# Performance work log

Hardware: AMD Instinct MI355X
Metric: run time of the kernel (lower is better)

Reference implementation:

```python
import jax, jax.numpy as jnp
import numpy as np

B, S, D = 1, 2048, 2048
H, HD = 16, 128  # n_heads, head_dim
ROPE_BASE = 100000.0


def setup_inputs() -> dict:
    key = jax.random.key(0)
    k0, k1, k2 = jax.random.split(key, 3)
    x = jax.random.normal(k0, (B, S, D), jnp.float32)
    # real RoPE table: (seq_len, head_dim//2, 2) holding (cos, sin)
    inv_freq = 1.0 / (ROPE_BASE ** (np.arange(0, HD, 2, dtype=np.float64) / HD))
    t = np.arange(S, dtype=np.float64)[:, None] * inv_freq[None, :]
    freqs_cis = jnp.asarray(np.stack([np.cos(t), np.sin(t)], axis=-1), jnp.float32)
    input_pos = jnp.arange(S, dtype=jnp.int32)
    Wqkv = jax.random.normal(k1, (D, 3 * D), jnp.float32) * (D ** -0.5)
    bqkv = jnp.zeros((3 * D,), jnp.float32)
    Wdense = jax.random.normal(k2, (D, D), jnp.float32) * (D ** -0.5)
    bdense = jnp.zeros((D,), jnp.float32)
    return {"x": x, "freqs_cis": freqs_cis, "input_pos": input_pos,
            "Wqkv": Wqkv, "bqkv": bqkv, "Wdense": Wdense, "bdense": bdense}


def apply_rotary_emb(x, freqs_cis):
    # x: [B, S, H, HD]; freqs_cis: [S, HD//2, 2]
    xs = x.reshape(*x.shape[:-1], -1, 2)  # [B,S,H,HD/2,2]
    fc = freqs_cis.reshape(1, xs.shape[1], 1, xs.shape[3], 2)
    out = jnp.stack([
        xs[..., 0] * fc[..., 0] - xs[..., 1] * fc[..., 1],
        xs[..., 1] * fc[..., 0] + xs[..., 0] * fc[..., 1],
    ], axis=-1)
    return out.reshape(x.shape).astype(x.dtype)


def reference(x, freqs_cis, input_pos, Wqkv, bqkv, Wdense, bdense):
    b, s, d = x.shape
    qkv = x @ Wqkv + bqkv                      # fused QKV projection
    q, k, v = jnp.split(qkv, 3, axis=-1)
    q = q.reshape(b, s, H, HD)
    k = k.reshape(b, s, H, HD)
    v = v.reshape(b, s, H, HD)
    q = apply_rotary_emb(q, freqs_cis)
    k = apply_rotary_emb(k, freqs_cis)
    # KV-cache update (cache batch = 1, max_seq = context_length)
    k_cache = jnp.zeros((1, S, H, HD), jnp.float32)
    v_cache = jnp.zeros((1, S, H, HD), jnp.float32)
    k_full = k_cache.at[:, input_pos].set(k)
    v_full = v_cache.at[:, input_pos].set(v)
    # causal SDPA in [B, H, S, HD] layout
    qh = q.transpose(0, 2, 1, 3)
    kh = k_full.transpose(0, 2, 1, 3)
    vh = v_full.transpose(0, 2, 1, 3)
    scale = HD ** -0.5
    scores = jnp.einsum('bhqd,bhkd->bhqk', qh, kh) * scale  # [B,H,S,S]
    causal = jnp.tril(jnp.ones((s, S), dtype=bool))
    scores = jnp.where(causal, scores, jnp.finfo(scores.dtype).min)
    attn = jax.nn.softmax(scores, axis=-1)
    ctx = jnp.einsum('bhqk,bhkd->bhqd', attn, vh)
    ctx = ctx.transpose(0, 2, 1, 3).reshape(b, s, d)
    return ctx @ Wdense + bdense
```

## Files before the change

kernel.cpp:

```cpp
#include <hip/hip_runtime.h>

#define S 2048
#define D 2048
#define H 16
#define HD 128
#define N3 6144

typedef __attribute__((ext_vector_type(8))) _Float16 f16x8;
typedef __attribute__((ext_vector_type(4))) float f32x4;
typedef unsigned short ushort_t;
typedef unsigned int uint_t;

__device__ __forceinline__ ushort_t f16_rne(float f) {
    _Float16 h = (_Float16)f;
    return __builtin_bit_cast(ushort_t, h);
}
__device__ __forceinline__ float f16_f32(ushort_t u) {
    return (float)__builtin_bit_cast(_Float16, u);
}

__global__ __launch_bounds__(256) void convert_f16_kernel(
    const float* __restrict__ in, ushort_t* __restrict__ hi)
{
    const int i = blockIdx.x * 256 + threadIdx.x;
    float4 v = ((const float4*)in)[i];
    ((ushort4*)hi)[i] = make_ushort4(f16_rne(v.x), f16_rne(v.y),
                                     f16_rne(v.z), f16_rne(v.w));
}

__global__ __launch_bounds__(256) void convert_t_kernel(
    const float* __restrict__ in, ushort_t* __restrict__ hi,
    int Kdim, int Ndim)
{
    __shared__ float tile[32][33];
    const int k0 = blockIdx.x * 32, n0 = blockIdx.y * 32;
    const int tx = threadIdx.x & 31, ty = threadIdx.x >> 5;
    #pragma unroll
    for (int r = 0; r < 4; r++)
        tile[ty + r * 8][tx] = in[(size_t)(k0 + ty + r * 8) * Ndim + n0 + tx];
    __syncthreads();
    const int n  = threadIdx.x >> 3;
    const int kc = (threadIdx.x & 7) * 4;
    const float v0 = tile[kc + 0][n], v1 = tile[kc + 1][n];
    const float v2 = tile[kc + 2][n], v3 = tile[kc + 3][n];
    const size_t off = (size_t)(n0 + n) * Kdim + k0 + kc;
    *(ushort4*)&hi[off] = make_ushort4(f16_rne(v0), f16_rne(v1),
                                       f16_rne(v2), f16_rne(v3));
}

__device__ __forceinline__ void gload16(const ushort_t* g, ushort_t* l) {
    __builtin_amdgcn_global_load_lds(
        (const __attribute__((address_space(1))) unsigned int*)g,
        (__attribute__((address_space(3))) unsigned int*)l, 16, 0, 0);
}

#define BK 32
#define TILE_ELEMS (128 * BK)

__device__ __forceinline__ void mm_core_1t(
    const ushort_t* __restrict__ Agh,
    const ushort_t* __restrict__ Bgh,
    const int K, ushort_t* lds, const int t, f32x4 (&acc)[4][4])
{
    const int lane = t & 63;
    const int wv   = t >> 6;
    const int lrow = lane >> 2;
    const int lk   = (lane & 3) * 8;
    const int quad = lane >> 4;
    const int lr   = lane & 15;
    const int wm   = (wv & 1) * 64;
    const int wn   = (wv >> 1) * 64;

    const int r0  = wv * 16;
    const int lo0 = r0 * BK;
    const int lo1 = (r0 + 64) * BK;

    auto stage = [&](int k0, int buf) {
        ushort_t* base = lds + buf * 2 * TILE_ELEMS;
        ushort_t* As_h = base;
        ushort_t* Bs_h = base + TILE_ELEMS;
        const size_t go0 = (size_t)(r0 + lrow) * K + k0 + lk;
        const size_t go1 = (size_t)(r0 + 64 + lrow) * K + k0 + lk;
        gload16(Agh + go0, As_h + lo0);
        gload16(Agh + go1, As_h + lo1);
        gload16(Bgh + go0, Bs_h + lo0);
        gload16(Bgh + go1, Bs_h + lo1);
    };

    stage(0, 0);

    const int niter = K / BK;
    for (int it = 0; it < niter; it++) {
        const int cur = it & 1;
        __syncthreads();

        if (it + 1 < niter) stage((it + 1) * BK, cur ^ 1);

        ushort_t* base = lds + cur * 2 * TILE_ELEMS;
        ushort_t* As_h = base;
        ushort_t* Bs_h = base + TILE_ELEMS;

        f16x8 af[4], bf[4];
        #pragma unroll
        for (int i = 0; i < 4; i++) {
            af[i] = *(const f16x8*)&As_h[(wm + i * 16 + lr) * BK + quad * 8];
            bf[i] = *(const f16x8*)&Bs_h[(wn + i * 16 + lr) * BK + quad * 8];
        }
        #pragma unroll
        for (int mt = 0; mt < 4; mt++)
            #pragma unroll
            for (int nt = 0; nt < 4; nt++)
                acc[mt][nt] = __builtin_amdgcn_mfma_f32_16x16x32_f16(
                    af[mt], bf[nt], acc[mt][nt], 0, 0, 0);
    }
}

__global__ __launch_bounds__(256) void gemm_qkv_mfma(
    const ushort_t* __restrict__ xh,
    const ushort_t* __restrict__ Wth,
    const float* __restrict__ bias, const float* __restrict__ freqs,
    const int* __restrict__ input_pos,
    ushort_t* __restrict__ qhg, ushort_t* __restrict__ khg,
    ushort_t* __restrict__ vhg)
{
    __shared__ ushort_t lds[2 * 2 * TILE_ELEMS];
    const int t = threadIdx.x;
    const int col0 = blockIdx.x * 128;
    const int row0 = blockIdx.y * 128;

    f32x4 acc[4][4] = {};
    mm_core_1t(xh + (size_t)row0 * D,
               Wth + (size_t)col0 * D,
               D, lds, t, acc);

    const int lane = t & 63;
    const int quad = lane >> 4;
    const int lr   = lane & 15;
    const int wm = ((t >> 6) & 1) * 64;
    const int wn = ((t >> 6) >> 1) * 64;

    const int which = col0 >> 11;
    const int hh = (col0 & 2047) >> 7;

    if (which == 2) {
        ushort_t* vh_b = vhg + (size_t)hh * HD * S;
        #pragma unroll
        for (int nt = 0; nt < 4; nt++) {
            const int d = wn + nt * 16 + lr;
            const float bsc = bias[col0 + d];
            #pragma unroll
            for (int mt = 0; mt < 4; mt++) {
                #pragma unroll
                for (int reg = 0; reg < 4; reg++) {
                    const int m = row0 + wm + mt * 16 + quad * 4 + reg;
                    const float v = acc[mt][nt][reg] + bsc;
                    const int pos = input_pos[m];
                    vh_b[(size_t)d * S + pos] = f16_rne(v);
                }
            }
        }
    } else {
        ushort_t* oh_b = ((which == 0) ? qhg : khg) + (size_t)hh * S * HD;
        #pragma unroll
        for (int nt = 0; nt < 4; nt++) {
            const int d = wn + nt * 16 + lr;
            const float bsc = bias[col0 + d];
            #pragma unroll
            for (int mt = 0; mt < 4; mt++) {
                #pragma unroll
                for (int reg = 0; reg < 4; reg++) {
                    const int m = row0 + wm + mt * 16 + quad * 4 + reg;
                    const float v = acc[mt][nt][reg] + bsc;
                    const float* fc = &freqs[((size_t)m * 64 + (d >> 1)) * 2];
                    const float c = fc[0], s = fc[1];
                    const float p = __shfl_xor(v, 1);
                    const float o = (d & 1) ? (v * c + p * s) : (v * c - p * s);
                    const ushort_t hv = f16_rne(o);
                    const int hp = __shfl_xor((int)hv, 1);
                    if (!(d & 1)) {
                        const int srow = (which == 0) ? m : input_pos[m];
                        *(uint_t*)&oh_b[(size_t)srow * HD + d] =
                            (uint_t)hv | ((uint_t)hp << 16);
                    }
                }
            }
        }
    }
}

__global__ __launch_bounds__(256, 2) void attn_mfma_kernel(
    const ushort_t* __restrict__ qhg, const ushort_t* __restrict__ khg,
    const ushort_t* __restrict__ vhg,
    float* __restrict__ Opart, float* __restrict__ MLpart)
{
    __shared__ ushort_t Khs[2][4096];
    __shared__ ushort_t Vhs[2][4096];
    __shared__ ushort_t Ps[64 * 32];

    const int bi   = blockIdx.x;
    const int h    = (bi & 7) + 8 * ((bi >> 3) & 1);
    const int half = (bi >> 4) & 1;
    const int qi   = bi >> 5;
    const int r = (h & 8) ? qi : (31 - qi);
    const int q0 = r * 64;
    const int nhalf = r + 1;
    const int kt0 = half * nhalf;
    const int kt1 = kt0 + nhalf;
    const int t = threadIdx.x;
    const int w = t >> 6, lane = t & 63;
    const int lr = lane & 15, quad = lane >> 4;

    const size_t qrow = (size_t)h * S + q0 + w * 16 + lr;
    f16x8 qf[4];
    #pragma unroll
    for (int ks = 0; ks < 4; ks++)
        qf[ks] = *(const f16x8*)&qhg[qrow * HD + ks * 32 + quad * 8];

    const ushort_t* kh_b = khg + (size_t)h * S * HD;
    const ushort_t* vh_b = vhg + (size_t)h * HD * S;

    const int keyq = lane >> 2;
    const int sub  = lane & 3;

    auto stage = [&](int kt, int buf) {
        const int k0 = kt * 32;
        #pragma unroll
        for (int hf = 0; hf < 2; hf++) {
            const size_t ksrc = (size_t)(k0 + hf * 16 + keyq) * HD + w * 32 + sub * 8;
            gload16(kh_b + ksrc, &Khs[buf][w * 1024 + hf * 512]);
            const int dim = w * 32 + hf * 16 + keyq;
            const size_t vsrc = (size_t)dim * S + k0 + sub * 8;
            gload16(vh_b + vsrc, &Vhs[buf][(w * 32 + hf * 16) * 32]);
        }
    };

    f32x4 O[8] = {};
    f32x4 Ol = {0.f, 0.f, 0.f, 0.f};
    float mrow[4];
    #pragma unroll
    for (int rr = 0; rr < 4; rr++) mrow[rr] = -1e30f;

    f16x8 onesv;
    #pragma unroll
    for (int i = 0; i < 8; i++) onesv[i] = (_Float16)1.0f;

    const float kSc = 0.08838834764831845f * 1.4426950408889634f;

    stage(kt0, 0);

    for (int kt = kt0; kt < kt1; kt++) {
        const int k0 = kt * 32;
        const int cur = (kt - kt0) & 1;
        __syncthreads();

        if (kt + 1 < kt1) stage(kt + 1, cur ^ 1);

        f32x4 sa[2];
        #pragma unroll
        for (int nt = 0; nt < 2; nt++) {
            f32x4 s = {0.f, 0.f, 0.f, 0.f};
            #pragma unroll
            for (int ks = 0; ks < 4; ks++) {
                f16x8 kf = *(const f16x8*)&Khs[cur][ks * 1024 + (nt * 16 + lr) * 32 + quad * 8];
                s = __builtin_amdgcn_mfma_f32_16x16x32_f16(qf[ks], kf, s, 0, 0, 0);
            }
            sa[nt] = s;
        }

        const int rowbase = q0 + w * 16 + quad * 4;
        const bool need_mask = (k0 + 31) > (q0 + w * 16);
        float alpha[4], pv0[4], pv1[4];
        #pragma unroll
        for (int rr = 0; rr < 4; rr++) {
            float z0 = sa[0][rr] * kSc;
            float z1 = sa[1][rr] * kSc;
            if (need_mask) {
                const int rowg = rowbase + rr;
                if (k0 + lr > rowg)      z0 = -1e30f;
                if (k0 + 16 + lr > rowg) z1 = -1e30f;
            }
            float rm = fmaxf(z0, z1);
            #pragma unroll
            for (int off = 1; off < 16; off <<= 1)
                rm = fmaxf(rm, __shfl_xor(rm, off));
            const float nm = fmaxf(mrow[rr], rm);
            alpha[rr] = exp2f(mrow[rr] - nm);
            pv0[rr] = exp2f(z0 - nm);
            pv1[rr] = exp2f(z1 - nm);
            mrow[rr] = nm;
        }

        #pragma unroll
        for (int rr = 0; rr < 4; rr++) {
            const int prow = (w * 16 + quad * 4 + rr) * 32;
            Ps[prow + lr]      = f16_rne(pv0[rr]);
            Ps[prow + 16 + lr] = f16_rne(pv1[rr]);
        }

        #pragma unroll
        for (int nt = 0; nt < 8; nt++)
            #pragma unroll
            for (int rr = 0; rr < 4; rr++)
                O[nt][rr] *= alpha[rr];
        #pragma unroll
        for (int rr = 0; rr < 4; rr++)
            Ol[rr] *= alpha[rr];
        const f16x8 pf = *(const f16x8*)&Ps[(w * 16 + lr) * 32 + quad * 8];
        #pragma unroll
        for (int nt = 0; nt < 8; nt++) {
            f16x8 vf = *(const f16x8*)&Vhs[cur][(nt * 16 + lr) * 32 + quad * 8];
            O[nt] = __builtin_amdgcn_mfma_f32_16x16x32_f16(pf, vf, O[nt], 0, 0, 0);
        }
        Ol = __builtin_amdgcn_mfma_f32_16x16x32_f16(pf, onesv, Ol, 0, 0, 0);
    }

    float* Ob = Opart + (size_t)bi * 64 * 128;
    #pragma unroll
    for (int rr = 0; rr < 4; rr++) {
        const int row = w * 16 + quad * 4 + rr;
        #pragma unroll
        for (int nt = 0; nt < 8; nt++)
            Ob[(size_t)row * 128 + nt * 16 + lr] = O[nt][rr];
        if (lr == 0) {
            MLpart[(size_t)bi * 128 + row * 2 + 0] = mrow[rr];
            MLpart[(size_t)bi * 128 + row * 2 + 1] = Ol[rr];
        }
    }
}

__global__ __launch_bounds__(128) void attn_combine_kernel(
    const float* __restrict__ Opart, const float* __restrict__ MLpart,
    ushort_t* __restrict__ ctxh)
{
    const int qt = blockIdx.x;
    const int h  = blockIdx.y;
    const int t  = threadIdx.x;
    const int b0 = h | (qt << 5);
    const int b1 = b0 | (1 << 4);
    const int r = (h & 8) ? qt : (31 - qt);
    const int q0 = r * 64;

    __shared__ float sc[64][2];
    if (t < 64) {
        const float m0 = MLpart[(size_t)b0 * 128 + t * 2 + 0];
        const float l0 = MLpart[(size_t)b0 * 128 + t * 2 + 1];
        const float m1 = MLpart[(size_t)b1 * 128 + t * 2 + 0];
        const float l1 = MLpart[(size_t)b1 * 128 + t * 2 + 1];
        const float m = fmaxf(m0, m1);
        const float a0 = exp2f(m0 - m), a1 = exp2f(m1 - m);
        const float inv = 1.0f / (l0 * a0 + l1 * a1);
        sc[t][0] = a0 * inv;
        sc[t][1] = a1 * inv;
    }
    __syncthreads();

    const float* O0 = Opart + (size_t)b0 * 64 * 128;
    const float* O1 = Opart + (size_t)b1 * 64 * 128;
    for (int row = 0; row < 64; row++) {
        const float o = O0[(size_t)row * 128 + t] * sc[row][0] +
                        O1[(size_t)row * 128 + t] * sc[row][1];
        ctxh[(size_t)(q0 + row) * D + h * HD + t] = f16_rne(o);
    }
}

__global__ __launch_bounds__(256) void gemm_dense_mfma(
    const ushort_t* __restrict__ Ah,
    const ushort_t* __restrict__ Wth,
    const float* __restrict__ bias, float* __restrict__ out)
{
    __shared__ ushort_t lds[2 * 2 * TILE_ELEMS];
    const int t = threadIdx.x;
    const int col0 = blockIdx.x * 128;
    const int row0 = blockIdx.y * 128;

    f32x4 acc[4][4] = {};
    mm_core_1t(Ah + (size_t)row0 * D,
               Wth + (size_t)col0 * D,
               D, lds, t, acc);

    const int lane = t & 63;
    const int quad = lane >> 4;
    const int lr   = lane & 15;
    const int wm = ((t >> 6) & 1) * 64;
    const int wn = ((t >> 6) >> 1) * 64;

    #pragma unroll
    for (int nt = 0; nt < 4; nt++) {
        const int n = col0 + wn + nt * 16 + lr;
        const float bsc = bias[n];
        #pragma unroll
        for (int mt = 0; mt < 4; mt++) {
            #pragma unroll
            for (int reg = 0; reg < 4; reg++) {
                const int m = row0 + wm + mt * 16 + quad * 4 + reg;
                const float o = acc[mt][nt][reg] + bsc;
                const float po = __shfl_xor(o, 1);
                if (!(n & 1))
                    *(float2*)&out[(size_t)m * D + n] = make_float2(o, po);
            }
        }
    }
}

__global__ __launch_bounds__(256) void gemm_qkv_kernel(
    const float* __restrict__ x, const float* __restrict__ W,
    const float* __restrict__ bias, const float* __restrict__ freqs,
    const int* __restrict__ input_pos,
    float* __restrict__ qb, float* __restrict__ kb, float* __restrict__ vb)
{
    __shared__ float As[16][68];
    __shared__ float Bs[16][64];
    const int bx = blockIdx.x;
    const int by = blockIdx.y;
    const int tid = threadIdx.x;
    const int tx = tid & 15, ty = tid >> 4;
    const int row0 = by * 64, col0 = bx * 64;
    const int am = tid >> 2;
    const int ak = (tid & 3) * 4;
    const int bk = tid >> 4;
    const int bn = (tid & 15) * 4;
    float acc[4][4] = {};
    for (int k0 = 0; k0 < D; k0 += 16) {
        float4 av = *(const float4*)&x[(size_t)(row0 + am) * D + k0 + ak];
        float4 bv = *(const float4*)&W[(size_t)(k0 + bk) * N3 + col0 + bn];
        __syncthreads();
        As[ak + 0][am] = av.x; As[ak + 1][am] = av.y;
        As[ak + 2][am] = av.z; As[ak + 3][am] = av.w;
        *(float4*)&Bs[bk][bn] = bv;
        __syncthreads();
        #pragma unroll
        for (int k = 0; k < 16; k++) {
            float4 a4 = *(const float4*)&As[k][ty * 4];
            float4 b4 = *(const float4*)&Bs[k][tx * 4];
            float a[4] = {a4.x, a4.y, a4.z, a4.w};
            float b[4] = {b4.x, b4.y, b4.z, b4.w};
            #pragma unroll
            for (int r = 0; r < 4; r++)
                #pragma unroll
                for (int c = 0; c < 4; c++)
                    acc[r][c] += a[r] * b[c];
        }
    }
    const int j0 = col0 + tx * 4;
    const int which = j0 >> 11;
    const int hh = (j0 & 2047) >> 7;
    const int d0 = j0 & 127;
    const float bv0 = bias[j0 + 0], bv1 = bias[j0 + 1];
    const float bv2 = bias[j0 + 2], bv3 = bias[j0 + 3];
    #pragma unroll
    for (int r = 0; r < 4; r++) {
        const int grow = row0 + ty * 4 + r;
        float v0 = acc[r][0] + bv0, v1 = acc[r][1] + bv1;
        float v2 = acc[r][2] + bv2, v3 = acc[r][3] + bv3;
        if (which == 2) {
            const int pos = input_pos[grow];
            float4 o4 = make_float4(v0, v1, v2, v3);
            *(float4*)&vb[((size_t)hh * S + pos) * HD + d0] = o4;
        } else {
            const float* fc = &freqs[((size_t)grow * 64 + (d0 >> 1)) * 2];
            float c0 = fc[0], s0 = fc[1], c1 = fc[2], s1 = fc[3];
            float o0 = v0 * c0 - v1 * s0, o1 = v1 * c0 + v0 * s0;
            float o2 = v2 * c1 - v3 * s1, o3 = v3 * c1 + v2 * s1;
            float4 o4 = make_float4(o0, o1, o2, o3);
            if (which == 0) {
                *(float4*)&qb[((size_t)hh * S + grow) * HD + d0] = o4;
            } else {
                const int pos = input_pos[grow];
                *(float4*)&kb[((size_t)hh * S + pos) * HD + d0] = o4;
            }
        }
    }
}

#define BQ 64
#define ABK 32
#define QSTR 132
#define KVSTR 132
#define PSTR 68

__global__ __launch_bounds__(256) void attn_kernel(
    const float* __restrict__ qb, const float* __restrict__ kb,
    const float* __restrict__ vb, float* __restrict__ ctx)
{
    __shared__ float Qs[BQ * QSTR];
    __shared__ float KV[ABK * KVSTR];
    __shared__ float Psf[ABK * PSTR];

    const int pa = blockIdx.x;
    const int h  = blockIdx.y;
    const int t  = threadIdx.x;
    const int ty = t >> 4, tx = t & 15;
    const int i0  = ty * 4;
    const int j0  = tx * 2;
    const int dd0 = tx * 8;
    const int lr = t >> 3;
    const int lc = (t & 7) * 4;

    const float* kbase = kb + (size_t)h * S * HD;
    const float* vbase = vb + (size_t)h * S * HD;
    const float kSc = 0.08838834764831845f * 1.4426950408889634f;

    for (int ph = 0; ph < 2; ph++) {
        const int r = (ph == 0) ? pa : 31 - pa;
        const int q0 = r * BQ;
        const int ntiles = 2 * r + 2;

        #pragma unroll
        for (int pp = 0; pp < 2; pp++) {
            const int iq = lr + pp * 32;
            const float* src = qb + ((size_t)h * S + q0 + iq) * HD;
            #pragma unroll
            for (int ch = 0; ch < 4; ch++)
                *(float4*)&Qs[iq * QSTR + lc + ch * 32] =
                    *(const float4*)&src[lc + ch * 32];
        }

        float O[4][8] = {};
        float m[4], l[4];
        #pragma unroll
        for (int rr = 0; rr < 4; rr++) { m[rr] = -1e30f; l[rr] = 0.f; }

        float4 kpref[4];
        #pragma unroll
        for (int ch = 0; ch < 4; ch++)
            kpref[ch] = *(const float4*)&kbase[(size_t)lr * HD + lc + ch * 32];

        __syncthreads();

        for (int kt = 0; kt < ntiles; kt++) {
            const int k0 = kt * ABK;

            #pragma unroll
            for (int ch = 0; ch < 4; ch++)
                *(float4*)&KV[lr * KVSTR + lc + ch * 32] = kpref[ch];
            __syncthreads();

            float4 vpref[4];
            #pragma unroll
            for (int ch = 0; ch < 4; ch++)
                vpref[ch] = *(const float4*)&vbase[(size_t)(k0 + lr) * HD + lc + ch * 32];

            float acc[4][2] = {};
            #pragma unroll 4
            for (int d0 = 0; d0 < HD; d0 += 4) {
                float4 ka = *(const float4*)&KV[(j0 + 0) * KVSTR + d0];
                float4 kb4 = *(const float4*)&KV[(j0 + 1) * KVSTR + d0];
                #pragma unroll
                for (int rr = 0; rr < 4; rr++) {
                    float4 q4 = *(const float4*)&Qs[(i0 + rr) * QSTR + d0];
                    acc[rr][0] += q4.x * ka.x + q4.y * ka.y + q4.z * ka.z + q4.w * ka.w;
                    acc[rr][1] += q4.x * kb4.x + q4.y * kb4.y + q4.z * kb4.z + q4.w * kb4.w;
                }
            }

            const bool need_mask = (k0 + ABK - 1) > q0;
            float p[4][2], alpha[4];
            #pragma unroll
            for (int rr = 0; rr < 4; rr++) {
                float z0 = acc[rr][0] * kSc;
                float z1 = acc[rr][1] * kSc;
                if (need_mask) {
                    if (k0 + j0 + 0 > q0 + i0 + rr) z0 = -1e30f;
                    if (k0 + j0 + 1 > q0 + i0 + rr) z1 = -1e30f;
                }
                float rmax = fmaxf(z0, z1);
                #pragma unroll
                for (int off = 1; off < 16; off <<= 1)
                    rmax = fmaxf(rmax, __shfl_xor(rmax, off, 16));
                const float nm = fmaxf(m[rr], rmax);
                alpha[rr] = exp2f(m[rr] - nm);
                p[rr][0] = exp2f(z0 - nm);
                p[rr][1] = exp2f(z1 - nm);
                float ts = p[rr][0] + p[rr][1];
                #pragma unroll
                for (int off = 1; off < 16; off <<= 1)
                    ts += __shfl_xor(ts, off, 16);
                l[rr] = l[rr] * alpha[rr] + ts;
                m[rr] = nm;
            }
            __syncthreads();

            #pragma unroll
            for (int ch = 0; ch < 4; ch++)
                *(float4*)&KV[lr * KVSTR + lc + ch * 32] = vpref[ch];
            *(float4*)&Psf[(j0 + 0) * PSTR + i0] =
                make_float4(p[0][0], p[1][0], p[2][0], p[3][0]);
            *(float4*)&Psf[(j0 + 1) * PSTR + i0] =
                make_float4(p[0][1], p[1][1], p[2][1], p[3][1]);
            if (kt + 1 < ntiles) {
                #pragma unroll
                for (int ch = 0; ch < 4; ch++)
                    kpref[ch] = *(const float4*)&kbase[(size_t)(k0 + ABK + lr) * HD + lc + ch * 32];
            }
            __syncthreads();

            #pragma unroll
            for (int rr = 0; rr < 4; rr++)
                #pragma unroll
                for (int c = 0; c < 8; c++)
                    O[rr][c] *= alpha[rr];
            #pragma unroll 4
            for (int j = 0; j < ABK; j++) {
                float4 pj = *(const float4*)&Psf[j * PSTR + i0];
                float4 v0 = *(const float4*)&KV[j * KVSTR + dd0];
                float4 v1 = *(const float4*)&KV[j * KVSTR + dd0 + 4];
                const float pr[4] = {pj.x, pj.y, pj.z, pj.w};
                const float vv[8] = {v0.x, v0.y, v0.z, v0.w, v1.x, v1.y, v1.z, v1.w};
                #pragma unroll
                for (int rr = 0; rr < 4; rr++)
                    #pragma unroll
                    for (int c = 0; c < 8; c++)
                        O[rr][c] += pr[rr] * vv[c];
            }
            __syncthreads();
        }

        #pragma unroll
        for (int rr = 0; rr < 4; rr++) {
            const float inv = 1.0f / l[rr];
            const int qg = q0 + i0 + rr;
            float4 o0 = make_float4(O[rr][0] * inv, O[rr][1] * inv,
                                    O[rr][2] * inv, O[rr][3] * inv);
            float4 o1 = make_float4(O[rr][4] * inv, O[rr][5] * inv,
                                    O[rr][6] * inv, O[rr][7] * inv);
            float* dst = &ctx[((size_t)qg * H + h) * HD + dd0];
            *(float4*)&dst[0] = o0;
            *(float4*)&dst[4] = o1;
        }
        __syncthreads();
    }
}

__global__ __launch_bounds__(256) void gemm_dense_kernel(
    const float* __restrict__ A, const float* __restrict__ W,
    const float* __restrict__ bias, float* __restrict__ out)
{
    __shared__ float As[16][68];
    __shared__ float Bs[16][64];
    const int bx = blockIdx.x;
    const int by = blockIdx.y;
    const int tid = threadIdx.x;
    const int tx = tid & 15, ty = tid >> 4;
    const int row0 = by * 64, col0 = bx * 64;
    const int am = tid >> 2;
    const int ak = (tid & 3) * 4;
    const int bk = tid >> 4;
    const int bn = (tid & 15) * 4;
    float acc[4][4] = {};
    for (int k0 = 0; k0 < D; k0 += 16) {
        float4 av = *(const float4*)&A[(size_t)(row0 + am) * D + k0 + ak];
        float4 bv = *(const float4*)&W[(size_t)(k0 + bk) * D + col0 + bn];
        __syncthreads();
        As[ak + 0][am] = av.x; As[ak + 1][am] = av.y;
        As[ak + 2][am] = av.z; As[ak + 3][am] = av.w;
        *(float4*)&Bs[bk][bn] = bv;
        __syncthreads();
        #pragma unroll
        for (int k = 0; k < 16; k++) {
            float4 a4 = *(const float4*)&As[k][ty * 4];
            float4 b4 = *(const float4*)&Bs[k][tx * 4];
            float a[4] = {a4.x, a4.y, a4.z, a4.w};
            float b[4] = {b4.x, b4.y, b4.z, b4.w};
            #pragma unroll
            for (int r = 0; r < 4; r++)
                #pragma unroll
                for (int c = 0; c < 4; c++)
                    acc[r][c] += a[r] * b[c];
        }
    }
    const int j0 = col0 + tx * 4;
    const float bv0 = bias[j0 + 0], bv1 = bias[j0 + 1];
    const float bv2 = bias[j0 + 2], bv3 = bias[j0 + 3];
    #pragma unroll
    for (int r = 0; r < 4; r++) {
        const int grow = row0 + ty * 4 + r;
        float4 o4 = make_float4(acc[r][0] + bv0, acc[r][1] + bv1,
                                acc[r][2] + bv2, acc[r][3] + bv3);
        *(float4*)&out[(size_t)grow * D + j0] = o4;
    }
}

extern "C" void kernel_launch(void* const* d_in, const int* in_sizes, int n_in,
                              void* d_out, int out_size, void* d_ws, size_t ws_size,
                              hipStream_t stream) {
    const float* x      = (const float*)d_in[0];
    const float* freqs  = (const float*)d_in[1];
    const int*   pos    = (const int*)d_in[2];
    const float* Wqkv   = (const float*)d_in[3];
    const float* bqkv   = (const float*)d_in[4];
    const float* Wdense = (const float*)d_in[5];
    const float* bdense = (const float*)d_in[6];
    float* out = (float*)d_out;

    const size_t nSD = (size_t)S * D;
    const size_t nW1 = (size_t)D * N3;
    const size_t nOP = (size_t)1024 * 64 * 128;
    const size_t nML = (size_t)1024 * 128;

    const size_t needed =
        (6 * nSD + nW1) * sizeof(ushort_t) + (nOP + nML) * sizeof(float);

    if (ws_size >= needed) {
        ushort_t* qh   = (ushort_t*)d_ws;
        ushort_t* kh   = qh + nSD;
        ushort_t* vh   = kh + nSD;
        ushort_t* ctxh = vh + nSD;
        ushort_t* xh   = ctxh + nSD;
        ushort_t* Wth  = xh + nSD;
        ushort_t* Wdth = Wth + nW1;
        float* Opart = (float*)(Wdth + nSD);
        float* MLpart = Opart + nOP;

        convert_f16_kernel<<<nSD / 4 / 256, 256, 0, stream>>>(x, xh);
        dim3 gt1(D / 32, N3 / 32);
        convert_t_kernel<<<gt1, 256, 0, stream>>>(Wqkv, Wth, D, N3);
        dim3 gt2(D / 32, D / 32);
        convert_t_kernel<<<gt2, 256, 0, stream>>>(Wdense, Wdth, D, D);

        dim3 g1(N3 / 128, S / 128);
        gemm_qkv_mfma<<<g1, 256, 0, stream>>>(xh, Wth, bqkv, freqs,
                                              pos, qh, kh, vh);
        attn_mfma_kernel<<<1024, 256, 0, stream>>>(qh, kh, vh,
                                                   Opart, MLpart);
        dim3 gc(32, H);
        attn_combine_kernel<<<gc, 128, 0, stream>>>(Opart, MLpart, ctxh);
        dim3 g3(D / 128, S / 128);
        gemm_dense_mfma<<<g3, 256, 0, stream>>>(ctxh, Wdth, bdense, out);
    } else {
        float* qb  = (float*)d_ws;
        float* kb  = qb + (size_t)H * S * HD;
        float* vb  = kb + (size_t)H * S * HD;
        float* ctx = vb + (size_t)H * S * HD;
        dim3 g1(N3 / 64, S / 64);
        gemm_qkv_kernel<<<g1, 256, 0, stream>>>(x, Wqkv, bqkv, freqs, pos, qb, kb, vb);
        dim3 g2(16, H);
        attn_kernel<<<g2, 256, 0, stream>>>(qb, kb, vb, ctx);
        dim3 g3(D / 64, S / 64);
        gemm_dense_kernel<<<g3, 256, 0, stream>>>(ctx, Wdense, bdense, out);
    }
}
```

Measured before the change: 362.4 us.

## Rewrite QKV GEMM with 256x256 tiles and explicit software-pipelined staging

Replaces the 128x128, 256-thread QKV projection GEMM with a 256x256-tile, 512-thread kernel. It uses a BK=64 K-step split into two halves, a double-buffered 128KB LDS, async global-to-LDS loads issued several phases ahead, and hand-placed vmcnt/lgkmcnt waits, barriers and s_setprio around the MFMA bursts. The goal is to raise arithmetic intensity per block and overlap global loads with MFMA work. The trade-off is that the grid shrinks to 192 blocks, fewer than the CU count, and the large LDS footprint limits each CU to one resident block. The bias and RoPE epilogue and the scatter to Q/K/V are kept as before, adapted to the larger tile.

```diff
diff --git a/kernel.cpp b/kernel.cpp
--- a/kernel.cpp
+++ b/kernel.cpp
@@ -54,6 +54,161 @@
         (__attribute__((address_space(3))) unsigned int*)l, 16, 0, 0);
 }
 
+__device__ __forceinline__ void vwait8() { asm volatile("s_waitcnt vmcnt(8)" ::: "memory"); }
+__device__ __forceinline__ void vwait4() { asm volatile("s_waitcnt vmcnt(4)" ::: "memory"); }
+__device__ __forceinline__ void vwait0() { asm volatile("s_waitcnt vmcnt(0)" ::: "memory"); }
+__device__ __forceinline__ void lwait0() { asm volatile("s_waitcnt lgkmcnt(0)" ::: "memory"); }
+
+#define QNT 32
+
+__global__ __launch_bounds__(512, 2) void gemm_qkv_mfma(
+    const ushort_t* __restrict__ xh,
+    const ushort_t* __restrict__ Wth,
+    const float* __restrict__ bias, const float* __restrict__ freqs,
+    const int* __restrict__ input_pos,
+    ushort_t* __restrict__ qhg, ushort_t* __restrict__ khg,
+    ushort_t* __restrict__ vhg)
+{
+    __shared__ ushort_t lds[65536];
+    const int t = threadIdx.x;
+    const int w = t >> 6, lane = t & 63;
+    const int lr = lane & 15, quad = lane >> 4;
+    const int wm = (w >> 2) * 128;
+    const int wn = (w & 3) * 64;
+
+    const int col0 = blockIdx.x * 256;
+    const int row0 = blockIdx.y * 256;
+    const ushort_t* At = xh + (size_t)row0 * D;
+    const ushort_t* Bt = Wth + (size_t)col0 * D;
+
+    const int srow = lane >> 2;
+    const int scol = (lane & 3) * 8;
+    const size_t goff0 = (size_t)((0 * 8 + w) * 16 + srow) * D + scol;
+    const size_t goff1 = (size_t)((1 * 8 + w) * 16 + srow) * D + scol;
+    const int ldst0 = (0 * 8 + w) * 512;
+    const int ldst1 = (1 * 8 + w) * 512;
+
+    auto stage = [&](int j, int Tt) {
+        const ushort_t* gb = (j & 1) ? Bt : At;
+        const int off = Tt * 64 + (j >> 1) * 32;
+        ushort_t* dst = lds + (Tt & 1) * 32768 + j * 8192;
+        gload16(gb + goff0 + off, dst + ldst0);
+        gload16(gb + goff1 + off, dst + ldst1);
+    };
+
+    f32x4 acc[8][4] = {};
+    const int aro = (wm + lr) * 32 + quad * 8;
+    const int bro = 8192 + (wn + lr) * 32 + quad * 8;
+
+    stage(0, 0); stage(1, 0); stage(2, 0); stage(3, 0);
+    stage(0, 1); stage(1, 1);
+    vwait4();
+    __builtin_amdgcn_sched_barrier(0);
+    __builtin_amdgcn_s_barrier();
+
+    f16x8 af[4], bf[4];
+
+#define QPH(kk, mtg, RDB, DOSTAGE, SJ, ST, WAITN)                          \
+    {                                                                      \
+        const ushort_t* base = lds + (T & 1) * 32768 + (kk) * 16384;       \
+        _Pragma("unroll")                                                  \
+        for (int i = 0; i < 4; i++)                                        \
+            af[i] = *(const f16x8*)&base[aro + ((mtg) * 4 + i) * 512];     \
+        if (RDB) {                                                         \
+            _Pragma("unroll")                                              \
+            for (int n = 0; n < 4; n++)                                    \
+                bf[n] = *(const f16x8*)&base[bro + n * 512];               \
+        }                                                                  \
+        if (DOSTAGE) stage(SJ, ST);                                        \
+        __builtin_amdgcn_s_barrier();                                      \
+        lwait0();                                                          \
+        __builtin_amdgcn_sched_barrier(0);                                 \
+        __builtin_amdgcn_s_setprio(1);                                     \
+        _Pragma("unroll")                                                  \
+        for (int i = 0; i < 4; i++)                                        \
+            _Pragma("unroll")                                              \
+            for (int n = 0; n < 4; n++)                                    \
+                acc[(mtg) * 4 + i][n] =                                    \
+                    __builtin_amdgcn_mfma_f32_16x16x32_f16(                \
+                        af[i], bf[n], acc[(mtg) * 4 + i][n], 0, 0, 0);     \
+        __builtin_amdgcn_s_setprio(0);                                     \
+        WAITN;                                                             \
+        __builtin_amdgcn_s_barrier();                                      \
+    }
+
+    for (int T = 0; T < QNT - 2; T++) {
+        QPH(0, 0, true,  true, 2, T + 1, );
+        QPH(0, 1, false, true, 3, T + 1, vwait8());
+        QPH(1, 0, true,  true, 0, T + 2, );
+        QPH(1, 1, false, true, 1, T + 2, vwait8());
+    }
+    {
+        const int T = QNT - 2;
+        QPH(0, 0, true,  true,  2, T + 1, );
+        QPH(0, 1, false, true,  3, T + 1, vwait8());
+        QPH(1, 0, true,  false, 0, 0, );
+        QPH(1, 1, false, false, 0, 0, vwait4());
+    }
+    {
+        const int T = QNT - 1;
+        QPH(0, 0, true,  false, 0, 0, );
+        QPH(0, 1, false, false, 0, 0, vwait0());
+        QPH(1, 0, true,  false, 0, 0, );
+        QPH(1, 1, false, false, 0, 0, );
+    }
+#undef QPH
+
+    const int which = col0 >> 11;
+    if (which == 2) {
+        #pragma unroll
+        for (int nt = 0; nt < 4; nt++) {
+            const int c = col0 + wn + nt * 16 + lr;
+            const int hh = (c & 2047) >> 7;
+            const int d = c & 127;
+            ushort_t* vh_b = vhg + (size_t)hh * HD * S;
+            const float bsc = bias[c];
+            #pragma unroll
+            for (int mt = 0; mt < 8; mt++) {
+                #pragma unroll
+                for (int reg = 0; reg < 4; reg++) {
+                    const int m = row0 + wm + mt * 16 + quad * 4 + reg;
+                    const float v = acc[mt][nt][reg] + bsc;
+                    vh_b[(size_t)d * S + input_pos[m]] = f16_rne(v);
+                }
+            }
+        }
+    } else {
+        ushort_t* ohg = (which == 0) ? qhg : khg;
+        #pragma unroll
+        for (int nt = 0; nt < 4; nt++) {
+            const int c = col0 + wn + nt * 16 + lr;
+            const int hh = (c & 2047) >> 7;
+            const int d = c & 127;
+            ushort_t* oh_b = ohg + (size_t)hh * S * HD;
+            const float bsc = bias[c];
+            #pragma unroll
+            for (int mt = 0; mt < 8; mt++) {
+                #pragma unroll
+                for (int reg = 0; reg < 4; reg++) {
+                    const int m = row0 + wm + mt * 16 + quad * 4 + reg;
+                    const float v = acc[mt][nt][reg] + bsc;
+                    const float* fc = &freqs[((size_t)m * 64 + (d >> 1)) * 2];
+                    const float cc = fc[0], ss = fc[1];
+                    const float p = __shfl_xor(v, 1);
+                    const float o = (d & 1) ? (v * cc + p * ss) : (v * cc - p * ss);
+                    const ushort_t hv = f16_rne(o);
+                    const int hp = __shfl_xor((int)hv, 1);
+                    if (!(d & 1)) {
+                        const int srowg = (which == 0) ? m : input_pos[m];
+                        *(uint_t*)&oh_b[(size_t)srowg * HD + d] =
+                            (uint_t)hv | ((uint_t)hp << 16);
+                    }
+                }
+            }
+        }
+    }
+}
+
 #define BK 32
 #define TILE_ELEMS (128 * BK)
 
@@ -112,79 +267,6 @@
             for (int nt = 0; nt < 4; nt++)
                 acc[mt][nt] = __builtin_amdgcn_mfma_f32_16x16x32_f16(
                     af[mt], bf[nt], acc[mt][nt], 0, 0, 0);
-    }
-}
-
-__global__ __launch_bounds__(256) void gemm_qkv_mfma(
-    const ushort_t* __restrict__ xh,
-    const ushort_t* __restrict__ Wth,
-    const float* __restrict__ bias, const float* __restrict__ freqs,
-    const int* __restrict__ input_pos,
-    ushort_t* __restrict__ qhg, ushort_t* __restrict__ khg,
-    ushort_t* __restrict__ vhg)
-{
-    __shared__ ushort_t lds[2 * 2 * TILE_ELEMS];
-    const int t = threadIdx.x;
-    const int col0 = blockIdx.x * 128;
-    const int row0 = blockIdx.y * 128;
-
-    f32x4 acc[4][4] = {};
-    mm_core_1t(xh + (size_t)row0 * D,
-               Wth + (size_t)col0 * D,
-               D, lds, t, acc);
-
-    const int lane = t & 63;
-    const int quad = lane >> 4;
-    const int lr   = lane & 15;
-    const int wm = ((t >> 6) & 1) * 64;
-    const int wn = ((t >> 6) >> 1) * 64;
-
-    const int which = col0 >> 11;
-    const int hh = (col0 & 2047) >> 7;
-
-    if (which == 2) {
-        ushort_t* vh_b = vhg + (size_t)hh * HD * S;
-        #pragma unroll
-        for (int nt = 0; nt < 4; nt++) {
-            const int d = wn + nt * 16 + lr;
-            const float bsc = bias[col0 + d];
-            #pragma unroll
-            for (int mt = 0; mt < 4; mt++) {
-                #pragma unroll
-                for (int reg = 0; reg < 4; reg++) {
-                    const int m = row0 + wm + mt * 16 + quad * 4 + reg;
-                    const float v = acc[mt][nt][reg] + bsc;
-                    const int pos = input_pos[m];
-                    vh_b[(size_t)d * S + pos] = f16_rne(v);
-                }
-            }
-        }
-    } else {
-        ushort_t* oh_b = ((which == 0) ? qhg : khg) + (size_t)hh * S * HD;
-        #pragma unroll
-        for (int nt = 0; nt < 4; nt++) {
-            const int d = wn + nt * 16 + lr;
-            const float bsc = bias[col0 + d];
-            #pragma unroll
-            for (int mt = 0; mt < 4; mt++) {
-                #pragma unroll
-                for (int reg = 0; reg < 4; reg++) {
-                    const int m = row0 + wm + mt * 16 + quad * 4 + reg;
-                    const float v = acc[mt][nt][reg] + bsc;
-                    const float* fc = &freqs[((size_t)m * 64 + (d >> 1)) * 2];
-                    const float c = fc[0], s = fc[1];
-                    const float p = __shfl_xor(v, 1);
-                    const float o = (d & 1) ? (v * c + p * s) : (v * c - p * s);
-                    const ushort_t hv = f16_rne(o);
-                    const int hp = __shfl_xor((int)hv, 1);
-                    if (!(d & 1)) {
-                        const int srow = (which == 0) ? m : input_pos[m];
-                        *(uint_t*)&oh_b[(size_t)srow * HD + d] =
-                            (uint_t)hv | ((uint_t)hp << 16);
-                    }
-                }
-            }
-        }
     }
 }
 
@@ -717,8 +799,8 @@
         dim3 gt2(D / 32, D / 32);
         convert_t_kernel<<<gt2, 256, 0, stream>>>(Wdense, Wdth, D, D);
 
-        dim3 g1(N3 / 128, S / 128);
-        gemm_qkv_mfma<<<g1, 256, 0, stream>>>(xh, Wth, bqkv, freqs,
+        dim3 g1(N3 / 256, S / 256);
+        gemm_qkv_mfma<<<g1, 512, 0, stream>>>(xh, Wth, bqkv, freqs,
                                               pos, qh, kh, vh);
         attn_mfma_kernel<<<1024, 256, 0, stream>>>(qh, kh, vh,
                                                    Opart, MLpart);
```

Measured after the change: 354.8 us. 1.02x faster.

## Replace GEMM core with deeper multi-stage pipelined LDS prefetch and explicit waitcnts

Applied to the files above, without the earlier changes.

The GEMM inner loop used by the QKV and dense projections is rewritten. It now uses a 64-wide K tile split into two 32-wide phases, with prefetch running two tiles ahead across a 64KB LDS double buffer. Explicit vmcnt/lgkmcnt waits, raw s_barrier calls, sched_barrier and setprio around the MFMA block aim to overlap global-to-LDS loads with compute and to cut the full __syncthreads cost. Launch bounds now request 2 blocks per CU. The risk is that 64KB of LDS per block limits occupancy, and the hand-placed waits must be exactly right to avoid races.

```diff
diff --git a/kernel.cpp b/kernel.cpp
--- a/kernel.cpp
+++ b/kernel.cpp
@@ -54,68 +54,94 @@
         (__attribute__((address_space(3))) unsigned int*)l, 16, 0, 0);
 }
 
-#define BK 32
-#define TILE_ELEMS (128 * BK)
-
-__device__ __forceinline__ void mm_core_1t(
-    const ushort_t* __restrict__ Agh,
-    const ushort_t* __restrict__ Bgh,
-    const int K, ushort_t* lds, const int t, f32x4 (&acc)[4][4])
-{
-    const int lane = t & 63;
-    const int wv   = t >> 6;
-    const int lrow = lane >> 2;
-    const int lk   = (lane & 3) * 8;
-    const int quad = lane >> 4;
-    const int lr   = lane & 15;
-    const int wm   = (wv & 1) * 64;
-    const int wn   = (wv >> 1) * 64;
-
-    const int r0  = wv * 16;
-    const int lo0 = r0 * BK;
-    const int lo1 = (r0 + 64) * BK;
-
-    auto stage = [&](int k0, int buf) {
-        ushort_t* base = lds + buf * 2 * TILE_ELEMS;
-        ushort_t* As_h = base;
-        ushort_t* Bs_h = base + TILE_ELEMS;
-        const size_t go0 = (size_t)(r0 + lrow) * K + k0 + lk;
-        const size_t go1 = (size_t)(r0 + 64 + lrow) * K + k0 + lk;
-        gload16(Agh + go0, As_h + lo0);
-        gload16(Agh + go1, As_h + lo1);
-        gload16(Bgh + go0, Bs_h + lo0);
-        gload16(Bgh + go1, Bs_h + lo1);
+__device__ __forceinline__ void vwait8() { asm volatile("s_waitcnt vmcnt(8)" ::: "memory"); }
+__device__ __forceinline__ void vwait4() { asm volatile("s_waitcnt vmcnt(4)" ::: "memory"); }
+__device__ __forceinline__ void vwait0() { asm volatile("s_waitcnt vmcnt(0)" ::: "memory"); }
+__device__ __forceinline__ void lwait0() { asm volatile("s_waitcnt lgkmcnt(0)" ::: "memory"); }
+
+#define QNT 32
+
+__device__ __forceinline__ void mm_core_8ph(
+    const ushort_t* __restrict__ At, const ushort_t* __restrict__ Bt,
+    ushort_t* lds, const int t, f32x4 (&acc)[4][4])
+{
+    const int w = t >> 6, lane = t & 63;
+    const int lr = lane & 15, quad = lane >> 4;
+    const int wm = (w & 1) * 64;
+    const int wn = (w >> 1) * 64;
+
+    const int srow = lane >> 2;
+    const int scol = (lane & 3) * 8;
+    const size_t goff0 = (size_t)(w * 16 + srow) * D + scol;
+    const size_t goff1 = goff0 + (size_t)64 * D;
+    const int ldst0 = w * 512;
+    const int ldst1 = 2048 + w * 512;
+
+    auto stage = [&](int j, int Tt) {
+        const ushort_t* gb = (j & 1) ? Bt : At;
+        const size_t off = (size_t)Tt * 64 + (j >> 1) * 32;
+        ushort_t* dst = lds + (Tt & 1) * 16384 + j * 4096;
+        gload16(gb + goff0 + off, dst + ldst0);
+        gload16(gb + goff1 + off, dst + ldst1);
     };
 
-    stage(0, 0);
-
-    const int niter = K / BK;
-    for (int it = 0; it < niter; it++) {
-        const int cur = it & 1;
-        __syncthreads();
-
-        if (it + 1 < niter) stage((it + 1) * BK, cur ^ 1);
-
-        ushort_t* base = lds + cur * 2 * TILE_ELEMS;
-        ushort_t* As_h = base;
-        ushort_t* Bs_h = base + TILE_ELEMS;
-
-        f16x8 af[4], bf[4];
-        #pragma unroll
-        for (int i = 0; i < 4; i++) {
-            af[i] = *(const f16x8*)&As_h[(wm + i * 16 + lr) * BK + quad * 8];
-            bf[i] = *(const f16x8*)&Bs_h[(wn + i * 16 + lr) * BK + quad * 8];
-        }
-        #pragma unroll
-        for (int mt = 0; mt < 4; mt++)
-            #pragma unroll
-            for (int nt = 0; nt < 4; nt++)
-                acc[mt][nt] = __builtin_amdgcn_mfma_f32_16x16x32_f16(
-                    af[mt], bf[nt], acc[mt][nt], 0, 0, 0);
-    }
-}
-
-__global__ __launch_bounds__(256) void gemm_qkv_mfma(
+    const int aro = (wm + lr) * 32 + quad * 8;
+    const int bro = 4096 + (wn + lr) * 32 + quad * 8;
+
+    stage(0, 0); stage(1, 0); stage(2, 0); stage(3, 0);
+    stage(0, 1); stage(1, 1);
+    vwait4();
+    __builtin_amdgcn_sched_barrier(0);
+    __builtin_amdgcn_s_barrier();
+
+    f16x8 af[4], bf[4];
+
+#define PH(kk, DOSTAGE, ST, WAITN)                                         \
+    {                                                                      \
+        const ushort_t* base = lds + (T & 1) * 16384 + (kk) * 8192;        \
+        _Pragma("unroll")                                                  \
+        for (int i = 0; i < 4; i++)                                        \
+            af[i] = *(const f16x8*)&base[aro + i * 512];                   \
+        _Pragma("unroll")                                                  \
+        for (int n = 0; n < 4; n++)                                        \
+            bf[n] = *(const f16x8*)&base[bro + n * 512];                   \
+        if (DOSTAGE) {                                                     \
+            stage((kk) ? 0 : 2, ST);                                       \
+            stage((kk) ? 1 : 3, ST);                                       \
+        }                                                                  \
+        __builtin_amdgcn_s_barrier();                                      \
+        lwait0();                                                          \
+        __builtin_amdgcn_sched_barrier(0);                                 \
+        __builtin_amdgcn_s_setprio(1);                                     \
+        _Pragma("unroll")                                                  \
+        for (int i = 0; i < 4; i++)                                        \
+            _Pragma("unroll")                                              \
+            for (int n = 0; n < 4; n++)                                    \
+                acc[i][n] = __builtin_amdgcn_mfma_f32_16x16x32_f16(        \
+                    af[i], bf[n], acc[i][n], 0, 0, 0);                     \
+        __builtin_amdgcn_s_setprio(0);                                     \
+        WAITN;                                                             \
+        __builtin_amdgcn_s_barrier();                                      \
+    }
+
+    for (int T = 0; T < QNT - 2; T++) {
+        PH(0, true, T + 1, vwait8());
+        PH(1, true, T + 2, vwait8());
+    }
+    {
+        const int T = QNT - 2;
+        PH(0, true,  T + 1, vwait8());
+        PH(1, false, 0,     vwait4());
+    }
+    {
+        const int T = QNT - 1;
+        PH(0, false, 0, vwait0());
+        PH(1, false, 0, );
+    }
+#undef PH
+}
+
+__global__ __launch_bounds__(256, 2) void gemm_qkv_mfma(
     const ushort_t* __restrict__ xh,
     const ushort_t* __restrict__ Wth,
     const float* __restrict__ bias, const float* __restrict__ freqs,
@@ -123,21 +149,20 @@
     ushort_t* __restrict__ qhg, ushort_t* __restrict__ khg,
     ushort_t* __restrict__ vhg)
 {
-    __shared__ ushort_t lds[2 * 2 * TILE_ELEMS];
+    __shared__ ushort_t lds[32768];
     const int t = threadIdx.x;
     const int col0 = blockIdx.x * 128;
     const int row0 = blockIdx.y * 128;
 
     f32x4 acc[4][4] = {};
-    mm_core_1t(xh + (size_t)row0 * D,
-               Wth + (size_t)col0 * D,
-               D, lds, t, acc);
+    mm_core_8ph(xh + (size_t)row0 * D, Wth + (size_t)col0 * D, lds, t, acc);
 
     const int lane = t & 63;
     const int quad = lane >> 4;
     const int lr   = lane & 15;
-    const int wm = ((t >> 6) & 1) * 64;
-    const int wn = ((t >> 6) >> 1) * 64;
+    const int w = t >> 6;
+    const int wm = (w & 1) * 64;
+    const int wn = (w >> 1) * 64;
 
     const int which = col0 >> 11;
     const int hh = (col0 & 2047) >> 7;
@@ -154,8 +179,7 @@
                 for (int reg = 0; reg < 4; reg++) {
                     const int m = row0 + wm + mt * 16 + quad * 4 + reg;
                     const float v = acc[mt][nt][reg] + bsc;
-                    const int pos = input_pos[m];
-                    vh_b[(size_t)d * S + pos] = f16_rne(v);
+                    vh_b[(size_t)d * S + input_pos[m]] = f16_rne(v);
                 }
             }
         }
@@ -172,17 +196,55 @@
                     const int m = row0 + wm + mt * 16 + quad * 4 + reg;
                     const float v = acc[mt][nt][reg] + bsc;
                     const float* fc = &freqs[((size_t)m * 64 + (d >> 1)) * 2];
-                    const float c = fc[0], s = fc[1];
+                    const float cc = fc[0], ss = fc[1];
                     const float p = __shfl_xor(v, 1);
-                    const float o = (d & 1) ? (v * c + p * s) : (v * c - p * s);
+                    const float o = (d & 1) ? (v * cc + p * ss) : (v * cc - p * ss);
                     const ushort_t hv = f16_rne(o);
                     const int hp = __shfl_xor((int)hv, 1);
                     if (!(d & 1)) {
-                        const int srow = (which == 0) ? m : input_pos[m];
-                        *(uint_t*)&oh_b[(size_t)srow * HD + d] =
+                        const int srowg = (which == 0) ? m : input_pos[m];
+                        *(uint_t*)&oh_b[(size_t)srowg * HD + d] =
                             (uint_t)hv | ((uint_t)hp << 16);
                     }
                 }
+            }
+        }
+    }
+}
+
+__global__ __launch_bounds__(256, 2) void gemm_dense_mfma(
+    const ushort_t* __restrict__ Ah,
+    const ushort_t* __restrict__ Wth,
+    const float* __restrict__ bias, float* __restrict__ out)
+{
+    __shared__ ushort_t lds[32768];
+    const int t = threadIdx.x;
+    const int col0 = blockIdx.x * 128;
+    const int row0 = blockIdx.y * 128;
+
+    f32x4 acc[4][4] = {};
+    mm_core_8ph(Ah + (size_t)row0 * D, Wth + (size_t)col0 * D, lds, t, acc);
+
+    const int lane = t & 63;
+    const int quad = lane >> 4;
+    const int lr   = lane & 15;
+    const int w = t >> 6;
+    const int wm = (w & 1) * 64;
+    const int wn = (w >> 1) * 64;
+
+    #pragma unroll
+    for (int nt = 0; nt < 4; nt++) {
+        const int n = col0 + wn + nt * 16 + lr;
+        const float bsc = bias[n];
+        #pragma unroll
+        for (int mt = 0; mt < 4; mt++) {
+            #pragma unroll
+            for (int reg = 0; reg < 4; reg++) {
+                const int m = row0 + wm + mt * 16 + quad * 4 + reg;
+                const float o = acc[mt][nt][reg] + bsc;
+                const float po = __shfl_xor(o, 1);
+                if (!(n & 1))
+                    *(float2*)&out[(size_t)m * D + n] = make_float2(o, po);
             }
         }
     }
@@ -360,45 +422,6 @@
         const float o = O0[(size_t)row * 128 + t] * sc[row][0] +
                         O1[(size_t)row * 128 + t] * sc[row][1];
         ctxh[(size_t)(q0 + row) * D + h * HD + t] = f16_rne(o);
-    }
-}
-
-__global__ __launch_bounds__(256) void gemm_dense_mfma(
-    const ushort_t* __restrict__ Ah,
-    const ushort_t* __restrict__ Wth,
-    const float* __restrict__ bias, float* __restrict__ out)
-{
-    __shared__ ushort_t lds[2 * 2 * TILE_ELEMS];
-    const int t = threadIdx.x;
-    const int col0 = blockIdx.x * 128;
-    const int row0 = blockIdx.y * 128;
-
-    f32x4 acc[4][4] = {};
-    mm_core_1t(Ah + (size_t)row0 * D,
-               Wth + (size_t)col0 * D,
-               D, lds, t, acc);
-
-    const int lane = t & 63;
-    const int quad = lane >> 4;
-    const int lr   = lane & 15;
-    const int wm = ((t >> 6) & 1) * 64;
-    const int wn = ((t >> 6) >> 1) * 64;
-
-    #pragma unroll
-    for (int nt = 0; nt < 4; nt++) {
-        const int n = col0 + wn + nt * 16 + lr;
-        const float bsc = bias[n];
-        #pragma unroll
-        for (int mt = 0; mt < 4; mt++) {
-            #pragma unroll
-            for (int reg = 0; reg < 4; reg++) {
-                const int m = row0 + wm + mt * 16 + quad * 4 + reg;
-                const float o = acc[mt][nt][reg] + bsc;
-                const float po = __shfl_xor(o, 1);
-                if (!(n & 1))
-                    *(float2*)&out[(size_t)m * D + n] = make_float2(o, po);
-            }
-        }
     }
 }
 
```

New measurement: 340.7 us. 1.06x faster.
